# Optimization experiments

Hardware: AMD Instinct MI355X
Metric: run time of the kernel (lower is better)

Reference implementation:

```python
import jax, jax.numpy as jnp
import numpy as np

SCS = 15000.0          # subcarrier_spacing_hz
FS = 30720000.0        # sampling_freq_hz
FACTOR = 1.5           # ebno_to_snr_factor
MAX_CFO = 0.05
NUM_TAPS = 5
PAD = (NUM_TAPS - 1) // 2

B, N = 64, 131072


def setup_inputs() -> dict:
    key = jax.random.key(0)
    ks = jax.random.split(key, 8)
    return {
        "x_real": jax.random.normal(ks[0], (B, N), jnp.float32),
        "x_imag": jax.random.normal(ks[1], (B, N), jnp.float32),
        "ebno_db": jax.random.uniform(ks[2], (B,), jnp.float32),
        "cfo_u": jax.random.uniform(ks[3], (B, 1), jnp.float32),
        "taps_real": jax.random.normal(ks[4], (B, NUM_TAPS), jnp.float32),
        "taps_imag": jax.random.normal(ks[5], (B, NUM_TAPS), jnp.float32),
        "noise_real": jax.random.normal(ks[6], (B, N), jnp.float32),
        "noise_imag": jax.random.normal(ks[7], (B, N), jnp.float32),
    }


def _depthwise_conv(x, taps):
    # torch F.conv1d (cross-correlation) with groups=batch, padding=PAD.
    # x: [B, N], taps: [B, K] -> y[b, n] = sum_k taps[b, k] * xpad[b, n + k]
    xp = jnp.pad(x, ((0, 0), (PAD, PAD)))
    n = x.shape[1]
    return sum(taps[:, k:k + 1] * xp[:, k:k + n] for k in range(NUM_TAPS))


def _forward(x_real, x_imag, ebno_db, cfo_u, taps_real, taps_imag,
             noise_real, noise_imag):
    # --- Residual CFO: x * exp(i * 2*pi * delta_f * t) ---
    cfo_norm = (cfo_u * 2.0 - 1.0) * MAX_CFO            # [B, 1]
    delta_f = cfo_norm * SCS
    t = jnp.arange(x_real.shape[1], dtype=jnp.float32) / FS  # [N]
    phase = 2.0 * jnp.pi * delta_f * t                  # [B, N]
    c, s = jnp.cos(phase), jnp.sin(phase)
    xr = x_real * c - x_imag * s
    xi = x_real * s + x_imag * c
    # --- TDL fading: complex depthwise conv with per-sample taps ---
    yr = _depthwise_conv(xr, taps_real) - _depthwise_conv(xi, taps_imag)
    yi = _depthwise_conv(xr, taps_imag) + _depthwise_conv(xi, taps_real)
    # --- AWGN ---
    snr_db = ebno_db + 10.0 * jnp.log10(jnp.float32(FACTOR))  # [B]
    noise_std = jnp.sqrt(10.0 ** (-snr_db / 10.0))            # [B]
    # torch.randn_like(complex) has per-component std 1/sqrt(2); scaled by std/sqrt(2)
    scale = (noise_std / 2.0)[:, None]
    yr = yr + noise_real * scale
    yi = yi + noise_imag * scale
    return jnp.stack([yr, yi], axis=0)  # [2, B, N]


def reference(x_real, x_imag, ebno_db, cfo_u, taps_real, taps_imag,
              noise_real, noise_imag):
    return _forward(x_real, x_imag, ebno_db, cfo_u, taps_real, taps_imag,
                    noise_real, noise_imag)
```

## Files before the change

kernel.cpp:

```cpp
#include <hip/hip_runtime.h>
#include <math.h>

#define BB   64
#define NN   131072
#define KTAPS 5
#define TILE 1024
#define NTHREADS 256

#define ANG_PER_HZ 2.0453077171808549e-7f
#define EBNO_OFF   1.7609125905568124f
#define L2TEN_OVER20 0.16609640474436813f

__device__ __forceinline__ float4 rot_edge2(const float* __restrict__ xr,
                                            const float* __restrict__ xi,
                                            size_t rowoff, int idx, float ang,
                                            float sA, float cA) {
    float4 r = make_float4(0.0f, 0.0f, 0.0f, 0.0f);
    if (idx >= 0 && idx + 1 < NN) {
        float2 a = *reinterpret_cast<const float2*>(xr + rowoff + (size_t)idx);
        float2 b = *reinterpret_cast<const float2*>(xi + rowoff + (size_t)idx);
        float ss, cc;
        sincosf(ang * (float)idx, &ss, &cc);
        r.x = a.x * cc - b.x * ss;
        r.y = a.x * ss + b.x * cc;
        float cn = cc * cA - ss * sA;
        float sn = ss * cA + cc * sA;
        r.z = a.y * cn - b.y * sn;
        r.w = a.y * sn + b.y * cn;
    }
    return r;
}

__global__ __launch_bounds__(NTHREADS) void wc_kernel(
    const float* __restrict__ x_real,  const float* __restrict__ x_imag,
    const float* __restrict__ ebno_db, const float* __restrict__ cfo_u,
    const float* __restrict__ taps_real, const float* __restrict__ taps_imag,
    const float* __restrict__ noise_real, const float* __restrict__ noise_imag,
    float* __restrict__ out)
{
    const int b    = blockIdx.y;
    const int tid  = threadIdx.x;
    const int base = blockIdx.x * TILE + tid * 4;
    const int lane = tid & 63;
    const size_t rowoff = (size_t)b * NN;

    const float cfo     = cfo_u[b];
    const float delta_f = (cfo * 2.0f - 1.0f) * 0.05f * 15000.0f;
    const float ang     = delta_f * ANG_PER_HZ;
    const float snr     = ebno_db[b] + EBNO_OFF;
    const float scale   = 0.5f * exp2f(-snr * L2TEN_OVER20);

    float tr[KTAPS], ti[KTAPS];
#pragma unroll
    for (int k = 0; k < KTAPS; ++k) {
        tr[k] = taps_real[b * KTAPS + k];
        ti[k] = taps_imag[b * KTAPS + k];
    }

    const float4 xr4 = *reinterpret_cast<const float4*>(x_real + rowoff + base);
    const float4 xi4 = *reinterpret_cast<const float4*>(x_imag + rowoff + base);
    const float xr_[4] = {xr4.x, xr4.y, xr4.z, xr4.w};
    const float xi_[4] = {xi4.x, xi4.y, xi4.z, xi4.w};

    float sA, cA, s, c;
    sincosf(ang, &sA, &cA);
    sincosf(ang * (float)base, &s, &c);

    float wr[8], wi[8];
#pragma unroll
    for (int j = 0; j < 4; ++j) {
        wr[2 + j] = xr_[j] * c - xi_[j] * s;
        wi[2 + j] = xr_[j] * s + xi_[j] * c;
        float cn = c * cA - s * sA;
        float sn = s * cA + c * sA;
        c = cn; s = sn;
    }

    wr[0] = __shfl_up(wr[4], 1, 64);
    wr[1] = __shfl_up(wr[5], 1, 64);
    wi[0] = __shfl_up(wi[4], 1, 64);
    wi[1] = __shfl_up(wi[5], 1, 64);
    wr[6] = __shfl_down(wr[2], 1, 64);
    wr[7] = __shfl_down(wr[3], 1, 64);
    wi[6] = __shfl_down(wi[2], 1, 64);
    wi[7] = __shfl_down(wi[3], 1, 64);

    if (lane == 0) {
        float4 e = rot_edge2(x_real, x_imag, rowoff, base - 2, ang, sA, cA);
        wr[0] = e.x; wi[0] = e.y;
        wr[1] = e.z; wi[1] = e.w;
    }
    if (lane == 63) {
        float4 e = rot_edge2(x_real, x_imag, rowoff, base + 4, ang, sA, cA);
        wr[6] = e.x; wi[6] = e.y;
        wr[7] = e.z; wi[7] = e.w;
    }

    const float4 nr4 = *reinterpret_cast<const float4*>(noise_real + rowoff + base);
    const float4 ni4 = *reinterpret_cast<const float4*>(noise_imag + rowoff + base);
    const float nr_[4] = {nr4.x, nr4.y, nr4.z, nr4.w};
    const float ni_[4] = {ni4.x, ni4.y, ni4.z, ni4.w};

    float oyr[4], oyi[4];
#pragma unroll
    for (int j = 0; j < 4; ++j) {
        float ar = 0.0f, ai = 0.0f;
#pragma unroll
        for (int k = 0; k < KTAPS; ++k) {
            ar = fmaf(tr[k], wr[j + k], ar);
            ar = fmaf(-ti[k], wi[j + k], ar);
            ai = fmaf(ti[k], wr[j + k], ai);
            ai = fmaf(tr[k], wi[j + k], ai);
        }
        oyr[j] = fmaf(nr_[j], scale, ar);
        oyi[j] = fmaf(ni_[j], scale, ai);
    }

    float4 yr4 = make_float4(oyr[0], oyr[1], oyr[2], oyr[3]);
    float4 yi4 = make_float4(oyi[0], oyi[1], oyi[2], oyi[3]);
    *reinterpret_cast<float4*>(out + rowoff + base) = yr4;
    *reinterpret_cast<float4*>(out + (size_t)BB * NN + rowoff + base) = yi4;
}

extern "C" void kernel_launch(void* const* d_in, const int* in_sizes, int n_in,
                              void* d_out, int out_size, void* d_ws, size_t ws_size,
                              hipStream_t stream) {
    const float* x_real     = (const float*)d_in[0];
    const float* x_imag     = (const float*)d_in[1];
    const float* ebno_db    = (const float*)d_in[2];
    const float* cfo_u      = (const float*)d_in[3];
    const float* taps_real  = (const float*)d_in[4];
    const float* taps_imag  = (const float*)d_in[5];
    const float* noise_real = (const float*)d_in[6];
    const float* noise_imag = (const float*)d_in[7];

    dim3 grid(NN / TILE, BB);
    wc_kernel<<<grid, NTHREADS, 0, stream>>>(
        x_real, x_imag, ebno_db, cfo_u, taps_real, taps_imag,
        noise_real, noise_imag, (float*)d_out);
}
```

Measured before the change: 183.0 us.

## Load halo via neighbor float4 loads, drop shuffles, use nontemporal stores

Each thread now loads the left and right neighbouring float4 of x_real/x_imag and rotates all 8 halo samples itself. This replaces the cross-lane shuffles and the divergent edge-lane branch that called sincosf. Loads are issued up front, before the scalar setup, to expose memory parallelism. Output stores become nontemporal to avoid polluting the cache. The cost is three times as many x loads per thread, which should mostly hit in cache, plus a few extra rotations per thread.

```diff
diff --git a/kernel.cpp b/kernel.cpp
--- a/kernel.cpp
+++ b/kernel.cpp
@@ -11,25 +11,7 @@
 #define EBNO_OFF   1.7609125905568124f
 #define L2TEN_OVER20 0.16609640474436813f
 
-__device__ __forceinline__ float4 rot_edge2(const float* __restrict__ xr,
-                                            const float* __restrict__ xi,
-                                            size_t rowoff, int idx, float ang,
-                                            float sA, float cA) {
-    float4 r = make_float4(0.0f, 0.0f, 0.0f, 0.0f);
-    if (idx >= 0 && idx + 1 < NN) {
-        float2 a = *reinterpret_cast<const float2*>(xr + rowoff + (size_t)idx);
-        float2 b = *reinterpret_cast<const float2*>(xi + rowoff + (size_t)idx);
-        float ss, cc;
-        sincosf(ang * (float)idx, &ss, &cc);
-        r.x = a.x * cc - b.x * ss;
-        r.y = a.x * ss + b.x * cc;
-        float cn = cc * cA - ss * sA;
-        float sn = ss * cA + cc * sA;
-        r.z = a.y * cn - b.y * sn;
-        r.w = a.y * sn + b.y * cn;
-    }
-    return r;
-}
+typedef float f32x4 __attribute__((ext_vector_type(4)));
 
 __global__ __launch_bounds__(NTHREADS) void wc_kernel(
     const float* __restrict__ x_real,  const float* __restrict__ x_imag,
@@ -39,10 +21,23 @@
     float* __restrict__ out)
 {
     const int b    = blockIdx.y;
-    const int tid  = threadIdx.x;
-    const int base = blockIdx.x * TILE + tid * 4;
-    const int lane = tid & 63;
+    const int base = blockIdx.x * TILE + threadIdx.x * 4;
     const size_t rowoff = (size_t)b * NN;
+
+    const float* __restrict__ xr = x_real + rowoff;
+    const float* __restrict__ xi = x_imag + rowoff;
+
+    const int aL = (base == 0)       ? 0        : base - 4;
+    const int aR = (base == NN - 4)  ? NN - 4   : base + 4;
+
+    const float4 xrL = *reinterpret_cast<const float4*>(xr + aL);
+    const float4 xr0 = *reinterpret_cast<const float4*>(xr + base);
+    const float4 xrR = *reinterpret_cast<const float4*>(xr + aR);
+    const float4 xiL = *reinterpret_cast<const float4*>(xi + aL);
+    const float4 xi0 = *reinterpret_cast<const float4*>(xi + base);
+    const float4 xiR = *reinterpret_cast<const float4*>(xi + aR);
+    const float4 nr4 = *reinterpret_cast<const float4*>(noise_real + rowoff + base);
+    const float4 ni4 = *reinterpret_cast<const float4*>(noise_imag + rowoff + base);
 
     const float cfo     = cfo_u[b];
     const float delta_f = (cfo * 2.0f - 1.0f) * 0.05f * 15000.0f;
@@ -57,51 +52,37 @@
         ti[k] = taps_imag[b * KTAPS + k];
     }
 
-    const float4 xr4 = *reinterpret_cast<const float4*>(x_real + rowoff + base);
-    const float4 xi4 = *reinterpret_cast<const float4*>(x_imag + rowoff + base);
-    const float xr_[4] = {xr4.x, xr4.y, xr4.z, xr4.w};
-    const float xi_[4] = {xi4.x, xi4.y, xi4.z, xi4.w};
-
     float sA, cA, s, c;
     sincosf(ang, &sA, &cA);
-    sincosf(ang * (float)base, &s, &c);
+    sincosf(ang * (float)(base - 2), &s, &c);
+
+    const bool lok = (base != 0);
+    const bool rok = (base != NN - 4);
+
+    float ur[8], ui[8];
+    ur[0] = lok ? xrL.z : 0.0f;  ui[0] = lok ? xiL.z : 0.0f;
+    ur[1] = lok ? xrL.w : 0.0f;  ui[1] = lok ? xiL.w : 0.0f;
+    ur[2] = xr0.x;  ui[2] = xi0.x;
+    ur[3] = xr0.y;  ui[3] = xi0.y;
+    ur[4] = xr0.z;  ui[4] = xi0.z;
+    ur[5] = xr0.w;  ui[5] = xi0.w;
+    ur[6] = rok ? xrR.x : 0.0f;  ui[6] = rok ? xiR.x : 0.0f;
+    ur[7] = rok ? xrR.y : 0.0f;  ui[7] = rok ? xiR.y : 0.0f;
 
     float wr[8], wi[8];
 #pragma unroll
-    for (int j = 0; j < 4; ++j) {
-        wr[2 + j] = xr_[j] * c - xi_[j] * s;
-        wi[2 + j] = xr_[j] * s + xi_[j] * c;
+    for (int j = 0; j < 8; ++j) {
+        wr[j] = ur[j] * c - ui[j] * s;
+        wi[j] = ur[j] * s + ui[j] * c;
         float cn = c * cA - s * sA;
         float sn = s * cA + c * sA;
         c = cn; s = sn;
     }
 
-    wr[0] = __shfl_up(wr[4], 1, 64);
-    wr[1] = __shfl_up(wr[5], 1, 64);
-    wi[0] = __shfl_up(wi[4], 1, 64);
-    wi[1] = __shfl_up(wi[5], 1, 64);
-    wr[6] = __shfl_down(wr[2], 1, 64);
-    wr[7] = __shfl_down(wr[3], 1, 64);
-    wi[6] = __shfl_down(wi[2], 1, 64);
-    wi[7] = __shfl_down(wi[3], 1, 64);
-
-    if (lane == 0) {
-        float4 e = rot_edge2(x_real, x_imag, rowoff, base - 2, ang, sA, cA);
-        wr[0] = e.x; wi[0] = e.y;
-        wr[1] = e.z; wi[1] = e.w;
-    }
-    if (lane == 63) {
-        float4 e = rot_edge2(x_real, x_imag, rowoff, base + 4, ang, sA, cA);
-        wr[6] = e.x; wi[6] = e.y;
-        wr[7] = e.z; wi[7] = e.w;
-    }
-
-    const float4 nr4 = *reinterpret_cast<const float4*>(noise_real + rowoff + base);
-    const float4 ni4 = *reinterpret_cast<const float4*>(noise_imag + rowoff + base);
     const float nr_[4] = {nr4.x, nr4.y, nr4.z, nr4.w};
     const float ni_[4] = {ni4.x, ni4.y, ni4.z, ni4.w};
 
-    float oyr[4], oyi[4];
+    f32x4 yr4, yi4;
 #pragma unroll
     for (int j = 0; j < 4; ++j) {
         float ar = 0.0f, ai = 0.0f;
@@ -112,14 +93,12 @@
             ai = fmaf(ti[k], wr[j + k], ai);
             ai = fmaf(tr[k], wi[j + k], ai);
         }
-        oyr[j] = fmaf(nr_[j], scale, ar);
-        oyi[j] = fmaf(ni_[j], scale, ai);
+        yr4[j] = fmaf(nr_[j], scale, ar);
+        yi4[j] = fmaf(ni_[j], scale, ai);
     }
 
-    float4 yr4 = make_float4(oyr[0], oyr[1], oyr[2], oyr[3]);
-    float4 yi4 = make_float4(oyi[0], oyi[1], oyi[2], oyi[3]);
-    *reinterpret_cast<float4*>(out + rowoff + base) = yr4;
-    *reinterpret_cast<float4*>(out + (size_t)BB * NN + rowoff + base) = yi4;
+    __builtin_nontemporal_store(yr4, reinterpret_cast<f32x4*>(out + rowoff + base));
+    __builtin_nontemporal_store(yi4, reinterpret_cast<f32x4*>(out + (size_t)BB * NN + rowoff + base));
 }
 
 extern "C" void kernel_launch(void* const* d_in, const int* in_sizes, int n_in,
```

New measurement: 180.8 us. No clear change (-1.2%).
